# Optimization experiments

Measured on AMD Instinct MI355X. Metric: run time of the kernel, lower is better.

Reference implementation:

```python
import jax, jax.numpy as jnp
import jax.scipy.linalg as jsl
import numpy as np

N_DATA, Q, LT, M_IND = 8192, 6, 10, 256
CHUNK = 512
JITTER = 1e-6


def _hankel(v, L):
    # Sliding-window gather, [Nv-L+1, L*D]. Replaces the original one-hot
    # matmul (O(N^2 L D)) with the equivalent O(N L D) gather -- same values.
    Nv, D = v.shape
    idx = jnp.arange(Nv - L + 1)[:, None] + jnp.arange(L)[None, :]
    return v[idx].reshape(Nv - L + 1, L * D)


def _elbo(X_mean, X_var, Z, kern_var, kern_len, lik_var, Lt):
    Nt, Qd = X_mean.shape
    M = Z.shape[0]
    sf2 = kern_var[0]
    l2 = kern_len[0] ** 2
    sigma2 = lik_var[0]
    sigma = jnp.sqrt(sigma2)

    X_m = _hankel(X_mean[:Nt - 1], Lt)            # [Nw, Lt*Q]
    X_v = _hankel(X_var[:Nt - 1], Lt)
    X_mo, X_vo = X_mean[Lt:], X_var[Lt:]          # [Nw, Q]
    X_mb, X_vb = X_mean[:Lt], X_var[:Lt]          # [Lt, Q]
    Nw, D = X_m.shape

    # RBF Kuu over inducing points
    zz = jnp.sum((Z[:, None, :] - Z[None, :, :]) ** 2, -1)        # [M, M]
    Kuu = sf2 * jnp.exp(-0.5 * zz / l2) + JITTER * jnp.eye(M, dtype=X_m.dtype)

    # psi0 = sum_n eKdiag = Nw * sf2 for RBF
    psi0 = Nw * sf2

    # psi1 [Nw, M] and psi2 = sum_n eKzxKxz [M, M], streamed over chunks of n
    n_chunks = Nw // CHUNK
    Xm_c = X_m.reshape(n_chunks, CHUNK, D)
    Xv_c = X_v.reshape(n_chunks, CHUNK, D)

    def body(acc, xs):
        mu, S = xs                                                 # [C, D]
        # psi1: sf2 * prod_d (1+S/l2)^-1/2 * exp(-0.5 (mu-z)^2/(S+l2))
        d1 = S + l2
        q1 = -0.5 * jnp.sum((mu[:, None, :] - Z[None, :, :]) ** 2
                            / d1[:, None, :], -1)                  # [C, M]
        ld1 = -0.5 * jnp.sum(jnp.log1p(S / l2), 1)                 # [C]
        psi1_c = sf2 * jnp.exp(ld1[:, None] + q1)
        # psi2 exponent  -(mu - zbar)^2 / (2S + l2)  decomposed into einsums
        w = 1.0 / (2.0 * S + l2)                                   # [C, D]
        ld2 = -0.5 * jnp.sum(jnp.log1p(2.0 * S / l2), 1)           # [C]
        e1 = jnp.sum(w * mu * mu, 1)                               # [C]
        e2 = jnp.einsum('nd,md->nm', w * mu, Z)                    # [C, M]
        e3 = 0.25 * jnp.einsum('nd,md->nm', w, Z * Z)              # [C, M]
        e4 = 0.5 * jnp.einsum('nd,md,pd->nmp', w, Z, Z)            # [C, M, M]
        quad = (e1[:, None, None] - e2[:, :, None] - e2[:, None, :]
                + e3[:, :, None] + e3[:, None, :] + e4)
        acc = acc + jnp.sum(jnp.exp(ld2[:, None, None] - quad), 0)
        return acc, psi1_c

    acc, psi1_chunks = jax.lax.scan(body, jnp.zeros((M, M), X_m.dtype),
                                    (Xm_c, Xv_c))
    psi1 = psi1_chunks.reshape(Nw, M)
    psi2 = (sf2 ** 2) * jnp.exp(-zz / (4.0 * l2)) * acc            # [M, M]

    # collapsed-bound linear algebra chain
    L = jnp.linalg.cholesky(Kuu)
    A = jsl.solve_triangular(L, psi1.T, lower=True) / sigma        # [M, Nw]
    tmp = jsl.solve_triangular(L, psi2, lower=True)
    AAT = jsl.solve_triangular(L, tmp.T, lower=True) / sigma2
    B = AAT + jnp.eye(M, dtype=X_m.dtype)
    LB = jnp.linalg.cholesky(B)
    log_det_B = 2.0 * jnp.sum(jnp.log(jnp.diagonal(LB)))
    c = jsl.solve_triangular(LB, A @ X_mo, lower=True) / sigma     # [M, Q]

    two_pi = 2.0 * np.pi
    ent = 0.5 * jnp.sum(jnp.log(X_vo)) + Nw * Qd * 0.5 * np.log(two_pi)
    ent2 = -Lt * Qd * np.log(two_pi) - 0.5 * jnp.sum(X_mb ** 2 + X_vb)
    bound = -0.5 * Nw * Qd * jnp.log(two_pi * sigma2)
    bound += -0.5 / sigma2 * (jnp.sum(X_vo) + jnp.sum(X_mo ** 2))
    bound += -0.5 * Qd * (psi0 / sigma2 - jnp.trace(AAT))
    bound += -0.5 * Qd * log_det_B
    bound += 0.5 * jnp.sum(c ** 2)
    bound += ent + ent2
    return bound


def setup_inputs() -> dict:
    key = jax.random.key(0)
    k1, k2, k3 = jax.random.split(key, 3)
    X_mean = jax.random.normal(k1, (N_DATA + LT, Q), jnp.float32)
    # positive variational variances (positive-transformed Param)
    X_var = jax.random.uniform(k2, (N_DATA + LT, Q), jnp.float32) * 0.5 + 0.1
    Z = jax.random.normal(k3, (M_IND, LT * Q), jnp.float32)
    return {
        "X_mean": X_mean,
        "X_var": X_var,
        "Z": Z,
        "kern_var": jnp.ones((1,), jnp.float32),
        "kern_len": jnp.full((1,), 8.0, jnp.float32),  # ~sqrt(D) lengthscale
        "lik_var": jnp.full((1,), 0.1, jnp.float32),
        "Lt": LT,
    }


def reference(X_mean, X_var, Z, kern_var, kern_len, lik_var, Lt):
    return _elbo(X_mean, X_var, Z, kern_var, kern_len, lik_var, Lt)
```

## Files before the change

kernel.cpp:

```cpp
#include <hip/hip_runtime.h>
#include <math.h>

#define QD 6
#define LTC 10
#define NW 8192
#define NT (NW + LTC)
#define D60 60
#define MI 256
#define JITTER 1e-6f
#define LOG2E 1.4426950408889634f

typedef __attribute__((ext_vector_type(8))) short bf16x8;
typedef __attribute__((ext_vector_type(4))) float f32x4;

#define OFF_W      0
#define OFF_SLOG   524288
#define OFF_ACC    (OFF_SLOG + 2097152)
#define OFF_KUU    (OFF_ACC + 65536)
#define OFF_G      (OFF_KUU + 65536)
#define OFF_PSI2   (OFF_G + 65536)
#define OFF_RPART  (OFF_PSI2 + 65536)
#define OFF_R      (OFF_RPART + 786432)
#define OFF_SCAL   (OFF_R + 1536)
#define OFF_TI1    (OFF_SCAL + 16)
#define OFF_KT     OFF_SLOG
#define OFF_GT     (OFF_SLOG + 65536)

__device__ __forceinline__ ushort f2bf(float f) {
    union { float f; unsigned u; } x; x.f = f;
    unsigned r = x.u + 0x7fffu + ((x.u >> 16) & 1u);
    return (ushort)(r >> 16);
}
__device__ __forceinline__ float bf2f(ushort h) {
    return __uint_as_float(((unsigned)h) << 16);
}
__device__ __forceinline__ unsigned cvt_pk_bf16(float a, float b) {
    unsigned r;
    asm("v_cvt_pk_bf16_f32 %0, %1, %2" : "=v"(r) : "v"(a), "v"(b));
    return r;
}

__global__ __launch_bounds__(256) void k_reduce_x(const float* __restrict__ Xm,
                                                  const float* __restrict__ Xv,
                                                  float* __restrict__ scal) {
    float s0 = 0.f, s1 = 0.f, s2 = 0.f, s3 = 0.f;
    const int tot = NT * QD;
    for (int i = blockIdx.x * blockDim.x + threadIdx.x; i < tot; i += gridDim.x * blockDim.x) {
        float xm = Xm[i], xv = Xv[i];
        if (i >= LTC * QD) { s0 += xv; s1 += xm * xm; s2 += __logf(xv); }
        else { s3 += xm * xm + xv; }
    }
    #pragma unroll
    for (int o = 32; o; o >>= 1) {
        s0 += __shfl_down(s0, o); s1 += __shfl_down(s1, o);
        s2 += __shfl_down(s2, o); s3 += __shfl_down(s3, o);
    }
    __shared__ float red[4][4];
    const int t = threadIdx.x;
    if ((t & 63) == 0) { int w = t >> 6; red[0][w] = s0; red[1][w] = s1; red[2][w] = s2; red[3][w] = s3; }
    __syncthreads();
    if (t == 0) {
        float a0 = 0, a1 = 0, a2 = 0, a3 = 0;
        for (int w = 0; w < 4; ++w) { a0 += red[0][w]; a1 += red[1][w]; a2 += red[2][w]; a3 += red[3][w]; }
        unsafeAtomicAdd(&scal[0], a0); unsafeAtomicAdd(&scal[1], a1);
        unsafeAtomicAdd(&scal[2], a2); unsafeAtomicAdd(&scal[3], a3);
    }
}

__global__ __launch_bounds__(256) void k_prep(const float* __restrict__ Xm, const float* __restrict__ Xv,
                                              const float* __restrict__ Zg, const float* __restrict__ kvar,
                                              const float* __restrict__ klen,
                                              float* __restrict__ W, float* __restrict__ Slog,
                                              float* __restrict__ rpart) {
    __shared__ float Zt[D60][MI];
    __shared__ float4 quadS[16][D60];
    __shared__ float sldS[16][2];
    __shared__ float xmoS[16][QD];
    const int t = threadIdx.x;
    const float sf2 = kvar[0];
    const float l = klen[0];
    const float l2 = l * l;
    for (int idx = t; idx < D60 * MI; idx += 256) {
        int d = idx >> 8, m = idx & 255;
        Zt[d][m] = Zg[m * D60 + d];
    }
    const int n0 = blockIdx.x * 16;
    const int wv = t >> 6, lane = t & 63;
    #pragma unroll
    for (int i = 0; i < 4; ++i) {
        const int nn = wv * 4 + i;
        const int n = n0 + nn;
        float lt1 = 0.f, lt2 = 0.f, e1 = 0.f;
        if (lane < D60) {
            float S = Xv[n * QD + lane], mu = Xm[n * QD + lane];
            float w = 1.0f / (2.0f * S + l2);
            float invd1 = 1.0f / (S + l2);
            quadS[nn][lane] = make_float4(w * mu, w, invd1, mu);
            W[n * 64 + lane] = -0.5f * LOG2E * w;
            lt1 = __logf(1.0f + S / l2);
            lt2 = __logf(1.0f + 2.0f * S / l2);
            e1 = w * mu * mu;
        } else {
            W[n * 64 + lane] = 0.f;
        }
        if (lane < QD) xmoS[nn][lane] = Xm[n * QD + D60 + lane];
        #pragma unroll
        for (int o = 32; o; o >>= 1) {
            lt1 += __shfl_down(lt1, o); lt2 += __shfl_down(lt2, o); e1 += __shfl_down(e1, o);
        }
        if (lane == 0) { sldS[nn][0] = -0.5f * lt1; sldS[nn][1] = 0.5f * (-0.5f * lt2 - e1); }
    }
    __syncthreads();
    float r6[QD];
    #pragma unroll
    for (int q = 0; q < QD; ++q) r6[q] = 0.f;
    for (int nn = 0; nn < 16; ++nn) {
        const int n = n0 + nn;
        float e2 = 0.f, e3 = 0.f, q1 = 0.f;
        #pragma unroll 10
        for (int d = 0; d < D60; ++d) {
            float4 qd = quadS[nn][d];
            float z = Zt[d][t];
            e2 += qd.x * z;
            e3 += qd.y * z * z;
            float dm = qd.w - z;
            q1 += dm * dm * qd.z;
        }
        Slog[n * MI + t] = sldS[nn][1] + e2 - 0.25f * e3;
        float psi1 = sf2 * __expf(sldS[nn][0] - 0.5f * q1);
        #pragma unroll
        for (int q = 0; q < QD; ++q) r6[q] += psi1 * xmoS[nn][q];
    }
    #pragma unroll
    for (int q = 0; q < QD; ++q) rpart[(blockIdx.x * MI + t) * QD + q] = r6[q];
}

__global__ __launch_bounds__(256, 3) void k_acc(const float* __restrict__ Zg, const float* __restrict__ W,
                                                const float* __restrict__ Slog, float* __restrict__ acc,
                                                int* __restrict__ q) {
    __shared__ ushort Ah[128 * 64];
    __shared__ ushort Al[128 * 64];
    __shared__ float Wlds[64 * 64];
    __shared__ float saa[128], sbb[64];
    __shared__ int wksh;
    const int t = threadIdx.x;
    if (t == 0) {
        int xcc = (int)(__builtin_amdgcn_s_getreg((31 << 11) | 20)) & 7;
        int work = 0;
        #pragma unroll 1
        for (int a = 0; a < 8; ++a) {
            int p = (xcc + a) & 7;
            int tk = atomicAdd(&q[p], 1);
            if (tk < 96) { work = p * 96 + tk; break; }
        }
        wksh = work;
    }
    __syncthreads();
    const int wk = wksh;
    const int nc = wk / 6;
    const int tile = wk % 6;
    const int m0 = (tile < 4) ? 0 : 128;
    const int p0 = (tile < 4) ? tile * 64 : 128 + (tile - 4) * 64;
    const int lane = t & 63, wid = t >> 6;
    const int wr = wid >> 1, wc = wid & 1;
    const int sm = t & 127, kh = t >> 7;
    const int n0 = nc * 64;

    float zr[32];
    #pragma unroll
    for (int j = 0; j < 32; ++j) {
        int k = kh * 32 + j;
        zr[j] = (k < D60) ? Zg[(m0 + sm) * D60 + k] : 0.f;
        asm volatile("" : "+v"(zr[j]));
    }
    for (int idx = t; idx < 64 * 64; idx += 256)
        Wlds[idx] = W[n0 * 64 + idx];
    for (int idx = t; idx < 64 * 64; idx += 256) {
        int p = idx >> 6, k = idx & 63;
        float v = (k < D60) ? Zg[(p0 + p) * D60 + k] : 0.f;
        ushort hi = f2bf(v);
        ushort lo = f2bf(v - bf2f(hi));
        int byte = p * 128 + ((k * 2) ^ ((p & 7) << 4));
        *(ushort*)((char*)Ah + byte) = hi;
        *(ushort*)((char*)Al + byte) = lo;
    }
    __syncthreads();
    bf16x8 bh[2][2], bl[2][2];
    #pragma unroll
    for (int ct = 0; ct < 2; ++ct) {
        int p = 32 * wc + 16 * ct + (lane & 15);
        int swz = (p & 7) << 4;
        #pragma unroll
        for (int h = 0; h < 2; ++h) {
            int byte = p * 128 + ((((lane >> 4) * 16) + 64 * h) ^ swz);
            bh[ct][h] = *(const bf16x8*)((const char*)Ah + byte);
            bl[ct][h] = *(const bf16x8*)((const char*)Al + byte);
        }
    }

    float accr[4][2][4];
    #pragma unroll
    for (int a = 0; a < 4; ++a)
        #pragma unroll
        for (int b = 0; b < 2; ++b)
            #pragma unroll
            for (int c = 0; c < 4; ++c) accr[a][b][c] = 0.f;

    for (int nn = 0; nn < 64; ++nn) {
        const int n = n0 + nn;
        __syncthreads();
        {
            const float* wrow = Wlds + nn * 64 + kh * 32;
            float av[32];
            #pragma unroll
            for (int j = 0; j < 8; ++j) {
                float4 f = *(const float4*)(wrow + 4 * j);
                av[4 * j + 0] = f.x * zr[4 * j + 0];
                av[4 * j + 1] = f.y * zr[4 * j + 1];
                av[4 * j + 2] = f.z * zr[4 * j + 2];
                av[4 * j + 3] = f.w * zr[4 * j + 3];
            }
            unsigned pkh[16], pkl[16];
            #pragma unroll
            for (int j = 0; j < 16; ++j) {
                float v0 = av[2 * j], v1 = av[2 * j + 1];
                unsigned ph = cvt_pk_bf16(v0, v1);
                float h0 = __uint_as_float(ph << 16);
                float h1 = __uint_as_float(ph & 0xffff0000u);
                pkh[j] = ph;
                pkl[j] = cvt_pk_bf16(v0 - h0, v1 - h1);
            }
            #pragma unroll
            for (int cc = 0; cc < 4; ++cc) {
                int byte = sm * 128 + (((kh * 64) + cc * 16) ^ ((sm & 7) << 4));
                uint4 vh; vh.x = pkh[4 * cc]; vh.y = pkh[4 * cc + 1]; vh.z = pkh[4 * cc + 2]; vh.w = pkh[4 * cc + 3];
                uint4 vl; vl.x = pkl[4 * cc]; vl.y = pkl[4 * cc + 1]; vl.z = pkl[4 * cc + 2]; vl.w = pkl[4 * cc + 3];
                *(uint4*)((char*)Ah + byte) = vh;
                *(uint4*)((char*)Al + byte) = vl;
            }
            if (t < 128) saa[t] = LOG2E * Slog[n * MI + m0 + t];
            else if (t < 192) sbb[t - 128] = LOG2E * Slog[n * MI + p0 + (t - 128)];
        }
        __syncthreads();
        float sbv[2];
        #pragma unroll
        for (int ct = 0; ct < 2; ++ct) sbv[ct] = sbb[32 * wc + 16 * ct + (lane & 15)];
        #pragma unroll
        for (int rt = 0; rt < 4; ++rt) {
            int m = 64 * wr + 16 * rt + (lane & 15);
            int swz = (m & 7) << 4;
            bf16x8 ah0 = *(const bf16x8*)((const char*)Ah + m * 128 + (((lane >> 4) * 16) ^ swz));
            bf16x8 ah1 = *(const bf16x8*)((const char*)Ah + m * 128 + ((64 + (lane >> 4) * 16) ^ swz));
            bf16x8 al0 = *(const bf16x8*)((const char*)Al + m * 128 + (((lane >> 4) * 16) ^ swz));
            bf16x8 al1 = *(const bf16x8*)((const char*)Al + m * 128 + ((64 + (lane >> 4) * 16) ^ swz));
            float sav[4];
            int rbase = 64 * wr + 16 * rt + (lane >> 4) * 4;
            #pragma unroll
            for (int rr = 0; rr < 4; ++rr) sav[rr] = saa[rbase + rr];
            #pragma unroll
            for (int ct = 0; ct < 2; ++ct) {
                f32x4 d;
                #pragma unroll
                for (int rr = 0; rr < 4; ++rr) d[rr] = sav[rr] + sbv[ct];
                d = __builtin_amdgcn_mfma_f32_16x16x32_bf16(ah0, bh[ct][0], d, 0, 0, 0);
                d = __builtin_amdgcn_mfma_f32_16x16x32_bf16(ah1, bh[ct][1], d, 0, 0, 0);
                d = __builtin_amdgcn_mfma_f32_16x16x32_bf16(ah0, bl[ct][0], d, 0, 0, 0);
                d = __builtin_amdgcn_mfma_f32_16x16x32_bf16(ah1, bl[ct][1], d, 0, 0, 0);
                d = __builtin_amdgcn_mfma_f32_16x16x32_bf16(al0, bh[ct][0], d, 0, 0, 0);
                d = __builtin_amdgcn_mfma_f32_16x16x32_bf16(al1, bh[ct][1], d, 0, 0, 0);
                #pragma unroll
                for (int rr = 0; rr < 4; ++rr)
                    accr[rt][ct][rr] += exp2f(d[rr]);
            }
        }
    }
    #pragma unroll
    for (int rt = 0; rt < 4; ++rt)
        #pragma unroll
        for (int ct = 0; ct < 2; ++ct)
            #pragma unroll
            for (int rr = 0; rr < 4; ++rr) {
                int row = m0 + 64 * wr + 16 * rt + (lane >> 4) * 4 + rr;
                int col = p0 + 32 * wc + 16 * ct + (lane & 15);
                unsafeAtomicAdd(&acc[row * MI + col], accr[rt][ct][rr]);
            }
}

__global__ __launch_bounds__(256) void k_psi2(const float* __restrict__ Zg, const float* __restrict__ kvar,
                                              const float* __restrict__ klen, const float* __restrict__ lvar,
                                              const float* __restrict__ acc, float* __restrict__ psi2,
                                              float* __restrict__ Kuu, float* __restrict__ G) {
    __shared__ float zi[D60];
    const int i = blockIdx.x, j = threadIdx.x;
    if (j < D60) zi[j] = Zg[i * D60 + j];
    __syncthreads();
    const float sf2 = kvar[0];
    const float l = klen[0];
    const float l2 = l * l;
    const float sigma2 = lvar[0];
    float zz = 0.f;
    #pragma unroll 10
    for (int d = 0; d < D60; ++d) {
        float dz = zi[d] - Zg[j * D60 + d];
        zz += dz * dz;
    }
    float accv = (i < 128 || j >= 128) ? acc[i * MI + j] : acc[j * MI + i];
    float p2 = sf2 * sf2 * __expf(-zz / (4.f * l2)) * accv;
    psi2[i * MI + j] = p2;
    float kv = sf2 * __expf(-0.5f * zz / l2) + ((i == j) ? JITTER : 0.f);
    Kuu[i * MI + j] = kv;
    G[i * MI + j] = kv + p2 / sigma2;
}

__global__ void k_reduce_r(const float* __restrict__ rpart, float* __restrict__ r) {
    int idx = blockIdx.x * blockDim.x + threadIdx.x;
    float s = 0.f;
    for (int b = 0; b < 512; ++b) s += rpart[b * 1536 + idx];
    r[idx] = s;
}

__global__ __launch_bounds__(1024) void k_chol2(float* __restrict__ A0, float* __restrict__ A1,
                                                float* __restrict__ At0, float* __restrict__ At1,
                                                float* __restrict__ scal) {
    float* A  = blockIdx.x ? A1 : A0;
    float* At = blockIdx.x ? At1 : At0;
    float* ldout = scal + 5 + blockIdx.x;
    __shared__ float Pt[32][MI];
    __shared__ float red[16];
    const int t = threadIdx.x;
    for (int p = 0; p < MI; p += 32) {
        const int R = MI - p;
        for (int idx = t; idx < R * 32; idx += 1024) {
            int c = idx / R, rr = idx % R;
            Pt[c][rr] = A[(p + rr) * MI + (p + c)];
        }
        __syncthreads();
        for (int jj = 0; jj < 32; ++jj) {
            float dg = sqrtf(fmaxf(Pt[jj][jj], 1e-20f));
            float inv = 1.0f / dg;
            for (int rr = jj + 1 + t; rr < R; rr += 1024) Pt[jj][rr] *= inv;
            if (t == 0) Pt[jj][jj] = dg;
            __syncthreads();
            int ncols = 31 - jj;
            if (ncols > 0) {
                int rows = R - jj - 1;
                for (int idx = t; idx < rows * ncols; idx += 1024) {
                    int c = jj + 1 + idx / rows;
                    int rr = jj + 1 + idx % rows;
                    Pt[c][rr] -= Pt[jj][rr] * Pt[jj][c];
                }
            }
            __syncthreads();
        }
        for (int idx = t; idx < R * 32; idx += 1024) {
            int c = idx / R, rr = idx % R;
            float v = Pt[c][rr];
            A[(p + rr) * MI + (p + c)] = v;
            At[(p + c) * MI + (p + rr)] = v;
        }
        const int T = R - 32;
        if (T > 0) {
            const int BT = T >> 2;
            const int nb = BT * (BT + 1) / 2;
            for (int b = t; b < nb; b += 1024) {
                int br = (int)((sqrtf(8.0f * b + 1.0f) - 1.0f) * 0.5f);
                while ((br + 1) * (br + 2) / 2 <= b) ++br;
                while (br * (br + 1) / 2 > b) --br;
                int bc = b - br * (br + 1) / 2;
                int r0 = 32 + br * 4, c0 = 32 + bc * 4;
                float s[4][4];
                #pragma unroll
                for (int i = 0; i < 4; ++i)
                    #pragma unroll
                    for (int j = 0; j < 4; ++j) s[i][j] = 0.f;
                #pragma unroll 8
                for (int kk = 0; kk < 32; ++kk) {
                    float4 av = *(const float4*)(&Pt[kk][r0]);
                    float4 bv = *(const float4*)(&Pt[kk][c0]);
                    float aa[4] = {av.x, av.y, av.z, av.w};
                    float bb[4] = {bv.x, bv.y, bv.z, bv.w};
                    #pragma unroll
                    for (int i = 0; i < 4; ++i)
                        #pragma unroll
                        for (int j = 0; j < 4; ++j) s[i][j] += aa[i] * bb[j];
                }
                #pragma unroll
                for (int i = 0; i < 4; ++i)
                    #pragma unroll
                    for (int j = 0; j < 4; ++j)
                        A[(p + r0 + i) * MI + (p + c0 + j)] -= s[i][j];
            }
        }
        __syncthreads();
    }
    float lg = 0.f;
    if (t < MI) lg = __logf(A[t * MI + t]);
    #pragma unroll
    for (int o = 32; o; o >>= 1) lg += __shfl_down(lg, o);
    if ((t & 63) == 0) red[t >> 6] = lg;
    __syncthreads();
    if (t == 0) {
        float s = 0.f;
        for (int k = 0; k < 16; ++k) s += red[k];
        ldout[0] = 2.0f * s;
    }
}

template<int NQ, bool WTI>
__device__ __forceinline__ float tri_fwd(const float* __restrict__ At, float* __restrict__ Ti,
                                         int j0, float (&acc)[4][NQ]) {
    const int lane = threadIdx.x & 63;
    const int r0 = lane * 4;
    float invd[4];
    #pragma unroll
    for (int s = 0; s < 4; ++s) invd[s] = 1.0f / At[(r0 + s) * MI + (r0 + s)];
    float4 col[4];
    #pragma unroll
    for (int s = 0; s < 4; ++s) col[s] = *(const float4*)(At + (j0 + s) * MI + r0);
    float cs = 0.f;
    for (int i4 = j0; i4 < MI; i4 += 4) {
        float4 ncol[4];
        const bool more = (i4 + 4 < MI);
        #pragma unroll
        for (int s = 0; s < 4; ++s)
            ncol[s] = more ? *(const float4*)(At + (i4 + 4 + s) * MI + r0)
                           : make_float4(0.f, 0.f, 0.f, 0.f);
        #pragma unroll
        for (int S = 0; S < 4; ++S) {
            const int i = i4 + S;
            const int src = i >> 2;
            float xi[NQ];
            #pragma unroll
            for (int q = 0; q < NQ; ++q)
                xi[q] = __shfl(acc[S][q] * invd[S], src);
            if (WTI) {
                if (lane == src) {
                    #pragma unroll
                    for (int q = 0; q < NQ; ++q) Ti[i * MI + j0 + q] = xi[q];
                }
            }
            const float lv0 = col[S].x, lv1 = col[S].y, lv2 = col[S].z, lv3 = col[S].w;
            #pragma unroll
            for (int q = 0; q < NQ; ++q) {
                acc[0][q] -= lv0 * xi[q];
                acc[1][q] -= lv1 * xi[q];
                acc[2][q] -= lv2 * xi[q];
                acc[3][q] -= lv3 * xi[q];
                cs += xi[q] * xi[q];
            }
        }
        #pragma unroll
        for (int s = 0; s < 4; ++s) col[s] = ncol[s];
    }
    return cs;
}

__global__ __launch_bounds__(64) void k_trinvK(const float* __restrict__ At, float* __restrict__ Ti) {
    const int lane = threadIdx.x;
    const int j0 = blockIdx.x * 16;
    const int r0 = lane * 4;
    float acc[4][16];
    #pragma unroll
    for (int s = 0; s < 4; ++s)
        #pragma unroll
        for (int q = 0; q < 16; ++q)
            acc[s][q] = (r0 + s == j0 + q) ? 1.f : 0.f;
    tri_fwd<16, true>(At, Ti, j0, acc);
}

__global__ __launch_bounds__(256) void k_tracedot(const float* __restrict__ Ti, const float* __restrict__ psi2,
                                                  float* __restrict__ scal) {
    __shared__ float vsh[MI];
    __shared__ float red[4];
    const int k = blockIdx.x, t = threadIdx.x;
    vsh[t] = Ti[k * MI + t];
    __syncthreads();
    float vj = vsh[t];
    float s = 0.f;
    for (int i = 0; i <= k; ++i) s += vsh[i] * psi2[i * MI + t];
    s *= vj;
    #pragma unroll
    for (int o = 32; o; o >>= 1) s += __shfl_down(s, o);
    if ((t & 63) == 0) red[t >> 6] = s;
    __syncthreads();
    if (t == 0) unsafeAtomicAdd(&scal[4], red[0] + red[1] + red[2] + red[3]);
}

__global__ __launch_bounds__(64) void k_solveG_final(const float* __restrict__ GT, const float* __restrict__ r,
                                                     const float* __restrict__ scal,
                                                     const float* __restrict__ kvar,
                                                     const float* __restrict__ lvar, const int* __restrict__ ltp,
                                                     float* __restrict__ out) {
    const int lane = threadIdx.x;
    const int r0 = lane * 4;
    float acc[4][QD];
    #pragma unroll
    for (int s = 0; s < 4; ++s)
        #pragma unroll
        for (int q = 0; q < QD; ++q)
            acc[s][q] = r[(r0 + s) * QD + q];
    float cs = tri_fwd<QD, false>(GT, nullptr, 0, acc);
    if (lane == 0) {
        double csum = (double)cs;
        double sigma2 = (double)lvar[0];
        double sf2 = (double)kvar[0];
        double two_pi = 6.283185307179586;
        double Nw = (double)NW, Q = (double)QD;
        double psi0 = Nw * sf2;
        double trace_AAT = (double)scal[4] / sigma2;
        double logdetB = (double)scal[6] - (double)scal[5];
        double bound = -0.5 * Nw * Q * log(two_pi * sigma2);
        bound += -0.5 / sigma2 * ((double)scal[0] + (double)scal[1]);
        bound += -0.5 * Q * (psi0 / sigma2 - trace_AAT);
        bound += -0.5 * Q * logdetB;
        bound += 0.5 * csum / (sigma2 * sigma2);
        bound += 0.5 * (double)scal[2] + Nw * Q * 0.5 * log(two_pi);
        bound += -(double)ltp[0] * Q * log(two_pi) - 0.5 * (double)scal[3];
        out[0] = (float)bound;
    }
}

extern "C" void kernel_launch(void* const* d_in, const int* in_sizes, int n_in,
                              void* d_out, int out_size, void* d_ws, size_t ws_size,
                              hipStream_t stream) {
    (void)in_sizes; (void)n_in; (void)out_size; (void)ws_size;
    const float* Xm = (const float*)d_in[0];
    const float* Xv = (const float*)d_in[1];
    const float* Zg = (const float*)d_in[2];
    const float* kvar = (const float*)d_in[3];
    const float* klen = (const float*)d_in[4];
    const float* lvar = (const float*)d_in[5];
    const int* ltp = (const int*)d_in[6];
    float* ws = (float*)d_ws;
    float* W = ws + OFF_W;
    float* Slog = ws + OFF_SLOG;
    float* acc = ws + OFF_ACC;
    float* Kuu = ws + OFF_KUU;
    float* G = ws + OFF_G;
    float* psi2 = ws + OFF_PSI2;
    float* rpart = ws + OFF_RPART;
    float* r = ws + OFF_R;
    float* scal = ws + OFF_SCAL;
    float* Ti1 = ws + OFF_TI1;
    float* KT = ws + OFF_KT;
    float* GT = ws + OFF_GT;

    hipMemsetAsync(acc, 0, MI * MI * sizeof(float), stream);
    hipMemsetAsync(scal, 0, 16 * sizeof(float), stream);
    hipMemsetAsync(Ti1, 0, MI * MI * sizeof(float), stream);

    k_reduce_x<<<64, 256, 0, stream>>>(Xm, Xv, scal);
    k_prep<<<512, 256, 0, stream>>>(Xm, Xv, Zg, kvar, klen, W, Slog, rpart);
    k_acc<<<768, 256, 0, stream>>>(Zg, W, Slog, acc, (int*)(scal + 8));
    k_psi2<<<256, 256, 0, stream>>>(Zg, kvar, klen, lvar, acc, psi2, Kuu, G);
    k_reduce_r<<<6, 256, 0, stream>>>(rpart, r);
    k_chol2<<<2, 1024, 0, stream>>>(Kuu, G, KT, GT, scal);
    k_trinvK<<<16, 64, 0, stream>>>(KT, Ti1);
    k_tracedot<<<256, 256, 0, stream>>>(Ti1, psi2, scal);
    k_solveG_final<<<1, 64, 0, stream>>>(GT, r, scal, kvar, lvar, ltp, (float*)d_out);
}
```

Baseline: 774.1 us.

## Fuse small reductions into neighbouring kernels and restructure blocked Cholesky

Folds the X reduction and the acc zeroing into k_prep, and the rpart reduction into extra blocks of the psi2 kernel, which removes several launches and memsets. Slog loads in k_acc are prefetched one iteration ahead. The Cholesky switches to an LDL-style update that defers the sqrt and scaling, accumulates log-det per panel, and removes one barrier per column. The Ti1 memset is dropped and tracedot masks the upper entries instead, which assumes k_trinvK writes every entry it reads. The log-det stored in scal no longer carries the factor 2; sum of log d equals twice the sum of log sqrt(d), so the value is unchanged.

```diff
diff --git a/kernel.cpp b/kernel.cpp
--- a/kernel.cpp
+++ b/kernel.cpp
@@ -40,43 +40,41 @@
     return r;
 }
 
-__global__ __launch_bounds__(256) void k_reduce_x(const float* __restrict__ Xm,
-                                                  const float* __restrict__ Xv,
-                                                  float* __restrict__ scal) {
-    float s0 = 0.f, s1 = 0.f, s2 = 0.f, s3 = 0.f;
-    const int tot = NT * QD;
-    for (int i = blockIdx.x * blockDim.x + threadIdx.x; i < tot; i += gridDim.x * blockDim.x) {
-        float xm = Xm[i], xv = Xv[i];
-        if (i >= LTC * QD) { s0 += xv; s1 += xm * xm; s2 += __logf(xv); }
-        else { s3 += xm * xm + xv; }
-    }
-    #pragma unroll
-    for (int o = 32; o; o >>= 1) {
-        s0 += __shfl_down(s0, o); s1 += __shfl_down(s1, o);
-        s2 += __shfl_down(s2, o); s3 += __shfl_down(s3, o);
-    }
-    __shared__ float red[4][4];
-    const int t = threadIdx.x;
-    if ((t & 63) == 0) { int w = t >> 6; red[0][w] = s0; red[1][w] = s1; red[2][w] = s2; red[3][w] = s3; }
-    __syncthreads();
-    if (t == 0) {
-        float a0 = 0, a1 = 0, a2 = 0, a3 = 0;
-        for (int w = 0; w < 4; ++w) { a0 += red[0][w]; a1 += red[1][w]; a2 += red[2][w]; a3 += red[3][w]; }
-        unsafeAtomicAdd(&scal[0], a0); unsafeAtomicAdd(&scal[1], a1);
-        unsafeAtomicAdd(&scal[2], a2); unsafeAtomicAdd(&scal[3], a3);
-    }
-}
-
 __global__ __launch_bounds__(256) void k_prep(const float* __restrict__ Xm, const float* __restrict__ Xv,
                                               const float* __restrict__ Zg, const float* __restrict__ kvar,
                                               const float* __restrict__ klen,
                                               float* __restrict__ W, float* __restrict__ Slog,
-                                              float* __restrict__ rpart) {
+                                              float* __restrict__ rpart,
+                                              float* __restrict__ accz, float* __restrict__ scal) {
     __shared__ float Zt[D60][MI];
     __shared__ float4 quadS[16][D60];
     __shared__ float sldS[16][2];
     __shared__ float xmoS[16][QD];
+    __shared__ float redx[4][4];
     const int t = threadIdx.x;
+    if (t < 128) accz[blockIdx.x * 128 + t] = 0.f;
+    if (blockIdx.x < 64) {
+        float s0 = 0.f, s1 = 0.f, s2 = 0.f, s3 = 0.f;
+        const int tot = NT * QD;
+        for (int i = blockIdx.x * 256 + t; i < tot; i += 64 * 256) {
+            float xm = Xm[i], xv = Xv[i];
+            if (i >= LTC * QD) { s0 += xv; s1 += xm * xm; s2 += __logf(xv); }
+            else { s3 += xm * xm + xv; }
+        }
+        #pragma unroll
+        for (int o = 32; o; o >>= 1) {
+            s0 += __shfl_down(s0, o); s1 += __shfl_down(s1, o);
+            s2 += __shfl_down(s2, o); s3 += __shfl_down(s3, o);
+        }
+        if ((t & 63) == 0) { int w = t >> 6; redx[0][w] = s0; redx[1][w] = s1; redx[2][w] = s2; redx[3][w] = s3; }
+        __syncthreads();
+        if (t == 0) {
+            float a0 = 0, a1 = 0, a2 = 0, a3 = 0;
+            for (int w = 0; w < 4; ++w) { a0 += redx[0][w]; a1 += redx[1][w]; a2 += redx[2][w]; a3 += redx[3][w]; }
+            unsafeAtomicAdd(&scal[0], a0); unsafeAtomicAdd(&scal[1], a1);
+            unsafeAtomicAdd(&scal[2], a2); unsafeAtomicAdd(&scal[3], a3);
+        }
+    }
     const float sf2 = kvar[0];
     const float l = klen[0];
     const float l2 = l * l;
@@ -206,8 +204,16 @@
             #pragma unroll
             for (int c = 0; c < 4; ++c) accr[a][b][c] = 0.f;
 
+    float sn = 0.f;
+    if (t < 128) sn = Slog[n0 * MI + m0 + t];
+    else if (t < 192) sn = Slog[n0 * MI + p0 + (t - 128)];
     for (int nn = 0; nn < 64; ++nn) {
-        const int n = n0 + nn;
+        float scur = sn;
+        if (nn + 1 < 64) {
+            const int n1 = n0 + nn + 1;
+            if (t < 128) sn = Slog[n1 * MI + m0 + t];
+            else if (t < 192) sn = Slog[n1 * MI + p0 + (t - 128)];
+        }
         __syncthreads();
         {
             const float* wrow = Wlds + nn * 64 + kh * 32;
@@ -238,8 +244,8 @@
                 *(uint4*)((char*)Ah + byte) = vh;
                 *(uint4*)((char*)Al + byte) = vl;
             }
-            if (t < 128) saa[t] = LOG2E * Slog[n * MI + m0 + t];
-            else if (t < 192) sbb[t - 128] = LOG2E * Slog[n * MI + p0 + (t - 128)];
+            if (t < 128) saa[t] = LOG2E * scur;
+            else if (t < 192) sbb[t - 128] = LOG2E * scur;
         }
         __syncthreads();
         float sbv[2];
@@ -286,10 +292,20 @@
             }
 }
 
-__global__ __launch_bounds__(256) void k_psi2(const float* __restrict__ Zg, const float* __restrict__ kvar,
-                                              const float* __restrict__ klen, const float* __restrict__ lvar,
-                                              const float* __restrict__ acc, float* __restrict__ psi2,
-                                              float* __restrict__ Kuu, float* __restrict__ G) {
+__global__ __launch_bounds__(256) void k_psi2r(const float* __restrict__ Zg, const float* __restrict__ kvar,
+                                               const float* __restrict__ klen, const float* __restrict__ lvar,
+                                               const float* __restrict__ acc, float* __restrict__ psi2,
+                                               float* __restrict__ Kuu, float* __restrict__ G,
+                                               const float* __restrict__ rpart, float* __restrict__ r) {
+    if (blockIdx.x >= 256) {
+        int idx = (blockIdx.x - 256) * 256 + threadIdx.x;
+        if (idx < 1536) {
+            float s = 0.f;
+            for (int b = 0; b < 512; ++b) s += rpart[b * 1536 + idx];
+            r[idx] = s;
+        }
+        return;
+    }
     __shared__ float zi[D60];
     const int i = blockIdx.x, j = threadIdx.x;
     if (j < D60) zi[j] = Zg[i * D60 + j];
@@ -312,22 +328,15 @@
     G[i * MI + j] = kv + p2 / sigma2;
 }
 
-__global__ void k_reduce_r(const float* __restrict__ rpart, float* __restrict__ r) {
-    int idx = blockIdx.x * blockDim.x + threadIdx.x;
-    float s = 0.f;
-    for (int b = 0; b < 512; ++b) s += rpart[b * 1536 + idx];
-    r[idx] = s;
-}
-
 __global__ __launch_bounds__(1024) void k_chol2(float* __restrict__ A0, float* __restrict__ A1,
                                                 float* __restrict__ At0, float* __restrict__ At1,
                                                 float* __restrict__ scal) {
     float* A  = blockIdx.x ? A1 : A0;
     float* At = blockIdx.x ? At1 : At0;
-    float* ldout = scal + 5 + blockIdx.x;
     __shared__ float Pt[32][MI];
-    __shared__ float red[16];
+    __shared__ float dsh[32];
     const int t = threadIdx.x;
+    float lgacc = 0.f;
     for (int p = 0; p < MI; p += 32) {
         const int R = MI - p;
         for (int idx = t; idx < R * 32; idx += 1024) {
@@ -335,29 +344,29 @@
             Pt[c][rr] = A[(p + rr) * MI + (p + c)];
         }
         __syncthreads();
-        for (int jj = 0; jj < 32; ++jj) {
-            float dg = sqrtf(fmaxf(Pt[jj][jj], 1e-20f));
-            float inv = 1.0f / dg;
-            for (int rr = jj + 1 + t; rr < R; rr += 1024) Pt[jj][rr] *= inv;
-            if (t == 0) Pt[jj][jj] = dg;
+        for (int jj = 0; jj < 31; ++jj) {
+            const float invd = 1.0f / fmaxf(Pt[jj][jj], 1e-20f);
+            const int rows = R - jj - 1, ncols = 31 - jj;
+            for (int idx = t; idx < rows * ncols; idx += 1024) {
+                int c = jj + 1 + idx / rows;
+                int rr = jj + 1 + idx % rows;
+                Pt[c][rr] -= Pt[jj][rr] * (Pt[jj][c] * invd);
+            }
             __syncthreads();
-            int ncols = 31 - jj;
-            if (ncols > 0) {
-                int rows = R - jj - 1;
-                for (int idx = t; idx < rows * ncols; idx += 1024) {
-                    int c = jj + 1 + idx / rows;
-                    int rr = jj + 1 + idx % rows;
-                    Pt[c][rr] -= Pt[jj][rr] * Pt[jj][c];
-                }
-            }
-            __syncthreads();
+        }
+        if (t < 32) {
+            float d = fmaxf(Pt[t][t], 1e-20f);
+            dsh[t] = 1.0f / d;
+            lgacc += __logf(d);
         }
         for (int idx = t; idx < R * 32; idx += 1024) {
             int c = idx / R, rr = idx % R;
-            float v = Pt[c][rr];
-            A[(p + rr) * MI + (p + c)] = v;
-            At[(p + c) * MI + (p + rr)] = v;
-        }
+            if (rr >= c) {
+                float rs = rsqrtf(fmaxf(Pt[c][c], 1e-20f));
+                At[(p + c) * MI + (p + rr)] = Pt[c][rr] * rs;
+            }
+        }
+        __syncthreads();
         const int T = R - 32;
         if (T > 0) {
             const int BT = T >> 2;
@@ -375,10 +384,11 @@
                     for (int j = 0; j < 4; ++j) s[i][j] = 0.f;
                 #pragma unroll 8
                 for (int kk = 0; kk < 32; ++kk) {
+                    float idk = dsh[kk];
                     float4 av = *(const float4*)(&Pt[kk][r0]);
                     float4 bv = *(const float4*)(&Pt[kk][c0]);
                     float aa[4] = {av.x, av.y, av.z, av.w};
-                    float bb[4] = {bv.x, bv.y, bv.z, bv.w};
+                    float bb[4] = {bv.x * idk, bv.y * idk, bv.z * idk, bv.w * idk};
                     #pragma unroll
                     for (int i = 0; i < 4; ++i)
                         #pragma unroll
@@ -388,21 +398,16 @@
                 for (int i = 0; i < 4; ++i)
                     #pragma unroll
                     for (int j = 0; j < 4; ++j)
-                        A[(p + r0 + i) * MI + (p + c0 + j)] -= s[i][j];
+                        A[(p + r0 - 32 + 32 + i) * MI + (p + c0 + j)] -= s[i][j];
             }
         }
         __syncthreads();
     }
-    float lg = 0.f;
-    if (t < MI) lg = __logf(A[t * MI + t]);
-    #pragma unroll
-    for (int o = 32; o; o >>= 1) lg += __shfl_down(lg, o);
-    if ((t & 63) == 0) red[t >> 6] = lg;
-    __syncthreads();
-    if (t == 0) {
-        float s = 0.f;
-        for (int k = 0; k < 16; ++k) s += red[k];
-        ldout[0] = 2.0f * s;
+    if (t < 32) {
+        float v = lgacc;
+        #pragma unroll
+        for (int o = 16; o; o >>= 1) v += __shfl_down(v, o);
+        if (t == 0) scal[5 + blockIdx.x] = v;
     }
 }
 
@@ -475,7 +480,7 @@
     const int k = blockIdx.x, t = threadIdx.x;
     vsh[t] = Ti[k * MI + t];
     __syncthreads();
-    float vj = vsh[t];
+    float vj = (t <= k) ? vsh[t] : 0.f;
     float s = 0.f;
     for (int i = 0; i <= k; ++i) s += vsh[i] * psi2[i * MI + t];
     s *= vj;
@@ -545,15 +550,11 @@
     float* KT = ws + OFF_KT;
     float* GT = ws + OFF_GT;
 
-    hipMemsetAsync(acc, 0, MI * MI * sizeof(float), stream);
     hipMemsetAsync(scal, 0, 16 * sizeof(float), stream);
-    hipMemsetAsync(Ti1, 0, MI * MI * sizeof(float), stream);
-
-    k_reduce_x<<<64, 256, 0, stream>>>(Xm, Xv, scal);
-    k_prep<<<512, 256, 0, stream>>>(Xm, Xv, Zg, kvar, klen, W, Slog, rpart);
+
+    k_prep<<<512, 256, 0, stream>>>(Xm, Xv, Zg, kvar, klen, W, Slog, rpart, acc, scal);
     k_acc<<<768, 256, 0, stream>>>(Zg, W, Slog, acc, (int*)(scal + 8));
-    k_psi2<<<256, 256, 0, stream>>>(Zg, kvar, klen, lvar, acc, psi2, Kuu, G);
-    k_reduce_r<<<6, 256, 0, stream>>>(rpart, r);
+    k_psi2r<<<262, 256, 0, stream>>>(Zg, kvar, klen, lvar, acc, psi2, Kuu, G, rpart, r);
     k_chol2<<<2, 1024, 0, stream>>>(Kuu, G, KT, GT, scal);
     k_trinvK<<<16, 64, 0, stream>>>(KT, Ti1);
     k_tracedot<<<256, 256, 0, stream>>>(Ti1, psi2, scal);
```

New measurement: 825.0 us. 6.6% more time.
